# Kernel tuning notes

Hardware: AMD Instinct MI355X
Metric: run time of the kernel (lower is better)

The kernel has to match this reference:

```python
import jax, jax.numpy as jnp
import numpy as np

B, L, D, I = 64, 196, 2048, 512

def setup_inputs() -> dict:
    key = jax.random.key(0)
    ks = jax.random.split(key, 8)
    s_f = 1.0 / np.sqrt(D)
    s_h = 1.0 / np.sqrt(I)
    s_a = 1.0 / np.sqrt(I)
    return {
        "feature_vectors": jax.random.normal(ks[0], (B, L, D), dtype=jnp.float32),
        "hidden_state": jax.random.normal(ks[1], (B, I), dtype=jnp.float32),
        "W_f": jax.random.uniform(ks[2], (D, I), jnp.float32, -s_f, s_f),
        "b_f": jax.random.uniform(ks[3], (I,), jnp.float32, -s_f, s_f),
        "W_h": jax.random.uniform(ks[4], (I, I), jnp.float32, -s_h, s_h),
        "b_h": jax.random.uniform(ks[5], (I,), jnp.float32, -s_h, s_h),
        "W_a": jax.random.uniform(ks[6], (I, D), jnp.float32, -s_a, s_a),
        "b_a": jax.random.uniform(ks[7], (D,), jnp.float32, -s_a, s_a),
    }

def reference(feature_vectors, hidden_state, W_f, b_f, W_h, b_h, W_a, b_a):
    # fv: [B,L,D], hidden: [B,I]
    fv_shaped = jnp.einsum('bld,di->bli', feature_vectors, W_f) + b_f      # [B,L,I]
    hs_shaped = hidden_state @ W_h + b_h                                   # [B,I]
    e = jnp.einsum('bli,id->bld', fv_shaped + hs_shaped[:, None, :], W_a) + b_a  # [B,L,D]
    alpha = jax.nn.softmax(e, axis=1)                                      # softmax over L locations
    z = jnp.sum(alpha * feature_vectors, axis=1)                           # [B,D] (vectorized loop)
    return (z, alpha)
```

## Files before the change

### kernel.cpp

```cpp
#include <hip/hip_runtime.h>

#define B_ 64
#define L_ 196
#define D_ 2048
#define I_ 512
#define M_ (B_*L_)

typedef __attribute__((ext_vector_type(8))) short bf16x8;
typedef __attribute__((ext_vector_type(4))) float f32x4;
typedef unsigned short u16;

__device__ __forceinline__ u16 f2bf(float x){
  unsigned u = __float_as_uint(x);
  u += 0x7fffu + ((u >> 16) & 1u);
  return (u16)(u >> 16);
}

__device__ __forceinline__ void gld16(const void* g, void* l){
  __builtin_amdgcn_global_load_lds(
      (const __attribute__((address_space(1))) void*)g,
      (__attribute__((address_space(3))) void*)l, 16, 0, 0);
}

template<int N> __device__ __forceinline__ void wait_vm(){
  __builtin_amdgcn_s_waitcnt((N&15) | ((N&48)<<10) | (7<<4) | (15<<8));
}
__device__ __forceinline__ void wait_lgkm0(){
  __builtin_amdgcn_s_waitcnt(15 | (48<<10) | (7<<4));
}
__device__ __forceinline__ void bar(){
  asm volatile("" ::: "memory");
  __builtin_amdgcn_s_barrier();
  asm volatile("" ::: "memory");
}

__device__ __forceinline__ unsigned cvtpk(float a, float b){
  unsigned r;
  asm("v_cvt_pk_bf16_f32 %0, %1, %2" : "=v"(r) : "v"(a), "v"(b));
  return r;
}

__global__ void transpose_cvt_kernel(const float* __restrict__ in, u16* __restrict__ out, int R, int C){
  __shared__ float tile[32][33];
  int c0 = blockIdx.x*32, r0 = blockIdx.y*32;
  int tx = threadIdx.x, ty = threadIdx.y;
  for (int i=0;i<32;i+=8)
    tile[ty+i][tx] = in[(size_t)(r0+ty+i)*C + c0 + tx];
  __syncthreads();
  for (int i=0;i<32;i+=8)
    out[(size_t)(c0+ty+i)*R + r0 + tx] = f2bf(tile[tx][ty+i]);
}

__launch_bounds__(256)
__global__ void hs_kernel(const float* __restrict__ hidden, const float* __restrict__ Wh,
                          const float* __restrict__ bh, float* __restrict__ hs){
  __shared__ float red[4][64];
  const int nl = threadIdx.x & 63, kg = threadIdx.x >> 6;
  const int n = blockIdx.x*64 + nl, b = blockIdx.y;
  const float* hrow = hidden + b*I_;
  float a0=0.f, a1=0.f;
  #pragma unroll
  for (int k=kg*128; k<kg*128+128; k+=2){
    a0 = fmaf(hrow[k+0], Wh[(size_t)(k+0)*I_ + n], a0);
    a1 = fmaf(hrow[k+1], Wh[(size_t)(k+1)*I_ + n], a1);
  }
  red[kg][nl] = a0 + a1;
  __syncthreads();
  if (kg == 0)
    hs[b*I_ + n] = bh[n] + (red[0][nl]+red[1][nl]) + (red[2][nl]+red[3][nl]);
}

__launch_bounds__(256)
__global__ void gemm1_kernel(const float* __restrict__ A, const u16* __restrict__ Bt,
                             const float* __restrict__ bias, const float* __restrict__ hs,
                             u16* __restrict__ outb)
{
  constexpr int K = D_, BK = 64, NIT = K/BK;
  __shared__ __align__(16) u16 Als[2][128*64];
  __shared__ __align__(16) u16 Bls[2][64*64];

  const int tid = threadIdx.x, lane = tid&63, wave = tid>>6;
  const int lid = blockIdx.y*8 + blockIdx.x;
  const int wid = (lid & 7)*98 + (lid >> 3);
  const int m0 = (wid >> 3)*128, n0 = (wid & 7)*64;
  const int q = lane>>4, mr = lane&15;
  const int wm = (wave&1)*64, wn = (wave>>1)*32;

  const int a_r  = wave*32 + (lane>>4);
  const int a_kc = lane&15;
  const float* Aw = A + (size_t)(m0 + a_r)*K + a_kc*4;
  const int b_r  = wave*16 + (lane>>3);
  const int b_kc = lane&7;
  const u16* Bw = Bt + (size_t)(n0 + b_r)*K + b_kc*8;

  int awo[8], bwo[2];
  #pragma unroll
  for (int u=0;u<8;++u){
    int r = a_r + u*4;
    awo[u] = r*64 + (((a_kc>>1) ^ (r&7))*8) + (a_kc&1)*4;
  }
  #pragma unroll
  for (int v=0;v<2;++v){
    int r = b_r + v*8;
    bwo[v] = r*64 + ((b_kc ^ (r&7))*8);
  }

  int aro[2][4], bro[2][2];
  #pragma unroll
  for (int s=0;s<2;++s){
    #pragma unroll
    for (int i2=0;i2<4;++i2){
      int r = wm + i2*16 + mr;
      aro[s][i2] = r*64 + (((s*4+q) ^ (r&7))*8);
    }
    #pragma unroll
    for (int j=0;j<2;++j){
      int r = wn + j*16 + mr;
      bro[s][j] = r*64 + (((s*4+q) ^ (r&7))*8);
    }
  }

  f32x4 rA[8]; bf16x8 rB[2];
  f32x4 acc[4][2];
  #pragma unroll
  for (int i=0;i<4;++i)
    #pragma unroll
    for (int j=0;j<2;++j) acc[i][j] = (f32x4){0.f,0.f,0.f,0.f};

#define G1_LOAD(k0) { \
  _Pragma("unroll") \
  for (int u=0;u<8;++u) rA[u] = *(const f32x4*)(Aw + (size_t)(u*4)*K + (k0)); \
  _Pragma("unroll") \
  for (int v=0;v<2;++v) rB[v] = *(const bf16x8*)(Bw + (size_t)(v*8)*K + (k0)); }

#define G1_CVTWR(bi) { \
  u16* Ab_ = Als[bi]; u16* Bb_ = Bls[bi]; \
  _Pragma("unroll") \
  for (int u=0;u<8;++u){ \
    unsigned lo = cvtpk(rA[u][0], rA[u][1]); \
    unsigned hi = cvtpk(rA[u][2], rA[u][3]); \
    *(uint2*)(Ab_ + awo[u]) = make_uint2(lo, hi); \
  } \
  _Pragma("unroll") \
  for (int v=0;v<2;++v) *(bf16x8*)(Bb_ + bwo[v]) = rB[v]; }

  G1_LOAD(0)
  G1_CVTWR(0)
  G1_LOAD(BK)
  wait_lgkm0(); bar();

  for (int t=0; t<NIT; ++t){
    if (t+1 < NIT) G1_CVTWR((t+1)&1)
    if (t+2 < NIT) G1_LOAD((t+2)*BK)
    const u16* Ab = Als[t&1];
    const u16* Bb = Bls[t&1];
    #pragma unroll
    for (int s=0;s<2;++s){
      bf16x8 af[4], bg[2];
      #pragma unroll
      for (int i2=0;i2<4;++i2) af[i2] = *(const bf16x8*)(Ab + aro[s][i2]);
      #pragma unroll
      for (int j=0;j<2;++j)    bg[j]  = *(const bf16x8*)(Bb + bro[s][j]);
      #pragma unroll
      for (int i2=0;i2<4;++i2)
        #pragma unroll
        for (int j=0;j<2;++j)
          acc[i2][j] = __builtin_amdgcn_mfma_f32_16x16x32_bf16(af[i2], bg[j], acc[i2][j], 0,0,0);
    }
    wait_lgkm0();
    bar();
  }

  #pragma unroll
  for (int i2=0;i2<4;++i2){
    #pragma unroll
    for (int j=0;j<2;++j){
      int gcol = n0 + wn + j*16 + mr;
      float bcol = bias[gcol];
      #pragma unroll
      for (int r=0;r<4;++r){
        int grow = m0 + wm + i2*16 + q*4 + r;
        int batch = grow / L_;
        outb[(size_t)grow*I_ + gcol] = f2bf(acc[i2][j][r] + bcol + hs[batch*I_ + gcol]);
      }
    }
  }
#undef G1_LOAD
#undef G1_CVTWR
}

__launch_bounds__(256)
__global__ void gemm2_fused_kernel(const u16* __restrict__ T, const u16* __restrict__ Wa,
                                   const float* __restrict__ b_a, const float* __restrict__ fv,
                                   float* __restrict__ out)
{
  constexpr int K = I_, BK = 32, NIT = K/BK;
  __shared__ __align__(16) u16 Als[2][256*32];
  __shared__ __align__(16) u16 Bls[2][64*32];

  const int tid = threadIdx.x, lane = tid&63, wave = tid>>6;
  const int b = blockIdx.y, n0 = blockIdx.x*64;
  const int q = lane>>4, mr = lane&15;
  const int l16 = lane>>2, kc4 = (lane&3)^(l16&3);

  const u16* Ag[4]; int Alo[4];
  #pragma unroll
  for (int u=0;u<4;++u){
    int j = wave*4+u;
    int grow = b*L_ + j*16 + l16; if (grow > M_-1) grow = M_-1;
    Ag[u] = T + (size_t)grow*K + kc4*8; Alo[u] = j*512;
  }
  const u16* Bg = Wa + (size_t)(n0 + wave*16 + l16)*K + kc4*8;
  const int  Blo = wave*512;

  const int abase = mr*32 + ((q ^ (mr&3))*8);
  const int col  = n0 + wave*16 + mr;
  const int boff = (wave*16+mr)*32 + ((q ^ (mr&3))*8);

  f32x4 acc[13];
  #pragma unroll
  for (int i=0;i<13;i++) acc[i] = (f32x4){0,0,0,0};

  #pragma unroll
  for (int u=0;u<4;++u) gld16(Ag[u],    &Als[0][Alo[u]]);
  gld16(Bg,    &Bls[0][Blo]);
  #pragma unroll
  for (int u=0;u<4;++u) gld16(Ag[u]+BK, &Als[1][Alo[u]]);
  gld16(Bg+BK, &Bls[1][Blo]);

  for (int it=0; it<NIT; ++it){
    if (it+1<NIT) wait_vm<5>(); else wait_vm<0>();
    bar();
    const u16* Ab = Als[it&1];
    const u16* Bb = Bls[it&1];
    bf16x8 bg0 = *(const bf16x8*)(Bb + boff);
    bf16x8 af[13];
    #pragma unroll
    for (int i=0;i<13;++i) af[i] = *(const bf16x8*)(Ab + abase + i*512);
    wait_lgkm0();
    bar();
    if (it+2<NIT){
      int k0 = (it+2)*BK;
      #pragma unroll
      for (int u=0;u<4;++u) gld16(Ag[u]+k0, &Als[it&1][Alo[u]]);
      gld16(Bg+k0, &Bls[it&1][Blo]);
    }
    #pragma unroll
    for (int i=0;i<13;++i)
      acc[i] = __builtin_amdgcn_mfma_f32_16x16x32_bf16(af[i], bg0, acc[i], 0,0,0);
  }

  const bool v12 = (q == 0);
  float bc = b_a[col];
  #pragma unroll
  for (int i=0;i<13;++i)
    #pragma unroll
    for (int r=0;r<4;++r) acc[i][r] += bc;

  float m = -3.4e38f;
  #pragma unroll
  for (int i=0;i<12;++i)
    #pragma unroll
    for (int r=0;r<4;++r) m = fmaxf(m, acc[i][r]);
  if (v12)
    #pragma unroll
    for (int r=0;r<4;++r) m = fmaxf(m, acc[12][r]);
  m = fmaxf(m, __shfl_xor(m, 16));
  m = fmaxf(m, __shfl_xor(m, 32));

  float s = 0.f;
  #pragma unroll
  for (int i=0;i<12;++i)
    #pragma unroll
    for (int r=0;r<4;++r){ float e = __expf(acc[i][r]-m); acc[i][r] = e; s += e; }
  if (v12)
    #pragma unroll
    for (int r=0;r<4;++r){ float e = __expf(acc[12][r]-m); acc[12][r] = e; s += e; }
  s += __shfl_xor(s, 16);
  s += __shfl_xor(s, 32);
  float inv = 1.f/s;

  float* alpha = out + (size_t)B_*D_ + (size_t)b*L_*D_;
  const float* fvb = fv + (size_t)b*L_*D_;
  float z = 0.f;
  #pragma unroll
  for (int i=0;i<13;++i){
    if (i < 12 || v12){
      #pragma unroll
      for (int r=0;r<4;++r){
        int row = i*16 + q*4 + r;
        float a = acc[i][r] * inv;
        alpha[(size_t)row*D_ + col] = a;
        z = fmaf(a, fvb[(size_t)row*D_ + col], z);
      }
    }
  }
  z += __shfl_xor(z, 16);
  z += __shfl_xor(z, 32);
  if (q == 0) out[(size_t)b*D_ + col] = z;
}

extern "C" void kernel_launch(void* const* d_in, const int* in_sizes, int n_in,
                              void* d_out, int out_size, void* d_ws, size_t ws_size,
                              hipStream_t stream){
  (void)in_sizes; (void)n_in; (void)out_size; (void)ws_size;
  const float* fv     = (const float*)d_in[0];
  const float* hidden = (const float*)d_in[1];
  const float* W_f    = (const float*)d_in[2];
  const float* b_f    = (const float*)d_in[3];
  const float* W_h    = (const float*)d_in[4];
  const float* b_h    = (const float*)d_in[5];
  const float* W_a    = (const float*)d_in[6];
  const float* b_a    = (const float*)d_in[7];
  float* out = (float*)d_out;

  char* ws = (char*)d_ws;
  u16*   t_bf  = (u16*)ws;
  u16*   WfT   = (u16*)(ws + 12845056);
  u16*   WaT   = (u16*)(ws + 14942208);
  float* hsbuf = (float*)(ws + 17039360);

  transpose_cvt_kernel<<<dim3(I_/32, D_/32), dim3(32,8), 0, stream>>>(W_f, WfT, D_, I_);
  transpose_cvt_kernel<<<dim3(D_/32, I_/32), dim3(32,8), 0, stream>>>(W_a, WaT, I_, D_);
  hs_kernel<<<dim3(I_/64, B_), 256, 0, stream>>>(hidden, W_h, b_h, hsbuf);

  gemm1_kernel<<<dim3(8, M_/128), 256, 0, stream>>>(fv, WfT, b_f, hsbuf, t_bf);
  gemm2_fused_kernel<<<dim3(D_/64, B_), 256, 0, stream>>>(t_bf, WaT, b_a, fv, out);
}
```

Before: 313.1 us.

## Merge prep kernels into one launch and split gemm1 tile across eight waves

Folds the two weight transpose/convert launches and the hidden-state projection into a single prep kernel that dispatches on block index, removing two kernel launches. gemm1 now uses 512 threads (8 waves) per 128x64 tile, so each wave owns a 32x32 sub-tile and loads half as much per stage. This cuts per-thread registers and adds more waves to hide latency, at the cost of fewer MFMAs per wave between barriers and more barrier participants.

```diff
diff --git a/kernel.cpp b/kernel.cpp
--- a/kernel.cpp
+++ b/kernel.cpp
@@ -40,37 +40,47 @@
   return r;
 }
 
-__global__ void transpose_cvt_kernel(const float* __restrict__ in, u16* __restrict__ out, int R, int C){
+__launch_bounds__(256)
+__global__ void prep_kernel(const float* __restrict__ Wf, u16* __restrict__ WfT,
+                            const float* __restrict__ Wa, u16* __restrict__ WaT,
+                            const float* __restrict__ hidden, const float* __restrict__ Wh,
+                            const float* __restrict__ bh, float* __restrict__ hsbuf){
   __shared__ float tile[32][33];
-  int c0 = blockIdx.x*32, r0 = blockIdx.y*32;
-  int tx = threadIdx.x, ty = threadIdx.y;
-  for (int i=0;i<32;i+=8)
-    tile[ty+i][tx] = in[(size_t)(r0+ty+i)*C + c0 + tx];
-  __syncthreads();
-  for (int i=0;i<32;i+=8)
-    out[(size_t)(c0+ty+i)*R + r0 + tx] = f2bf(tile[tx][ty+i]);
-}
-
-__launch_bounds__(256)
-__global__ void hs_kernel(const float* __restrict__ hidden, const float* __restrict__ Wh,
-                          const float* __restrict__ bh, float* __restrict__ hs){
   __shared__ float red[4][64];
-  const int nl = threadIdx.x & 63, kg = threadIdx.x >> 6;
-  const int n = blockIdx.x*64 + nl, b = blockIdx.y;
-  const float* hrow = hidden + b*I_;
-  float a0=0.f, a1=0.f;
-  #pragma unroll
-  for (int k=kg*128; k<kg*128+128; k+=2){
-    a0 = fmaf(hrow[k+0], Wh[(size_t)(k+0)*I_ + n], a0);
-    a1 = fmaf(hrow[k+1], Wh[(size_t)(k+1)*I_ + n], a1);
-  }
-  red[kg][nl] = a0 + a1;
-  __syncthreads();
-  if (kg == 0)
-    hs[b*I_ + n] = bh[n] + (red[0][nl]+red[1][nl]) + (red[2][nl]+red[3][nl]);
-}
-
-__launch_bounds__(256)
+  const int bid = blockIdx.x, tid = threadIdx.x;
+  if (bid < 2048){
+    const float* in; u16* out; int R, C, id;
+    if (bid < 1024){ in = Wf; out = WfT; R = D_; C = I_; id = bid; }
+    else           { in = Wa; out = WaT; R = I_; C = D_; id = bid - 1024; }
+    const int nx = C/32;
+    const int c0 = (id % nx)*32, r0 = (id / nx)*32;
+    const int tx = tid & 31, ty = tid >> 5;
+    #pragma unroll
+    for (int i=0;i<32;i+=8)
+      tile[ty+i][tx] = in[(size_t)(r0+ty+i)*C + c0 + tx];
+    __syncthreads();
+    #pragma unroll
+    for (int i=0;i<32;i+=8)
+      out[(size_t)(c0+ty+i)*R + r0 + tx] = f2bf(tile[tx][ty+i]);
+  } else {
+    const int id = bid - 2048;
+    const int nl = tid & 63, kg = tid >> 6;
+    const int n = (id & 7)*64 + nl, b = id >> 3;
+    const float* hrow = hidden + b*I_;
+    float a0=0.f, a1=0.f;
+    #pragma unroll
+    for (int k=kg*128; k<kg*128+128; k+=2){
+      a0 = fmaf(hrow[k+0], Wh[(size_t)(k+0)*I_ + n], a0);
+      a1 = fmaf(hrow[k+1], Wh[(size_t)(k+1)*I_ + n], a1);
+    }
+    red[kg][nl] = a0 + a1;
+    __syncthreads();
+    if (kg == 0)
+      hsbuf[b*I_ + n] = bh[n] + (red[0][nl]+red[1][nl]) + (red[2][nl]+red[3][nl]);
+  }
+}
+
+__launch_bounds__(512)
 __global__ void gemm1_kernel(const float* __restrict__ A, const u16* __restrict__ Bt,
                              const float* __restrict__ bias, const float* __restrict__ hs,
                              u16* __restrict__ outb)
@@ -84,32 +94,28 @@
   const int wid = (lid & 7)*98 + (lid >> 3);
   const int m0 = (wid >> 3)*128, n0 = (wid & 7)*64;
   const int q = lane>>4, mr = lane&15;
-  const int wm = (wave&1)*64, wn = (wave>>1)*32;
-
-  const int a_r  = wave*32 + (lane>>4);
+  const int wm = (wave&3)*32, wn = (wave>>2)*32;
+
+  const int a_r  = wave*16 + (lane>>4);
   const int a_kc = lane&15;
   const float* Aw = A + (size_t)(m0 + a_r)*K + a_kc*4;
-  const int b_r  = wave*16 + (lane>>3);
+  const int b_r  = wave*8 + (lane>>3);
   const int b_kc = lane&7;
   const u16* Bw = Bt + (size_t)(n0 + b_r)*K + b_kc*8;
 
-  int awo[8], bwo[2];
-  #pragma unroll
-  for (int u=0;u<8;++u){
+  int awo[4];
+  #pragma unroll
+  for (int u=0;u<4;++u){
     int r = a_r + u*4;
     awo[u] = r*64 + (((a_kc>>1) ^ (r&7))*8) + (a_kc&1)*4;
   }
-  #pragma unroll
-  for (int v=0;v<2;++v){
-    int r = b_r + v*8;
-    bwo[v] = r*64 + ((b_kc ^ (r&7))*8);
-  }
-
-  int aro[2][4], bro[2][2];
+  const int bwo = b_r*64 + ((b_kc ^ (b_r&7))*8);
+
+  int aro[2][2], bro[2][2];
   #pragma unroll
   for (int s=0;s<2;++s){
     #pragma unroll
-    for (int i2=0;i2<4;++i2){
+    for (int i2=0;i2<2;++i2){
       int r = wm + i2*16 + mr;
       aro[s][i2] = r*64 + (((s*4+q) ^ (r&7))*8);
     }
@@ -120,29 +126,27 @@
     }
   }
 
-  f32x4 rA[8]; bf16x8 rB[2];
-  f32x4 acc[4][2];
-  #pragma unroll
-  for (int i=0;i<4;++i)
+  f32x4 rA[4]; bf16x8 rB;
+  f32x4 acc[2][2];
+  #pragma unroll
+  for (int i=0;i<2;++i)
     #pragma unroll
     for (int j=0;j<2;++j) acc[i][j] = (f32x4){0.f,0.f,0.f,0.f};
 
 #define G1_LOAD(k0) { \
   _Pragma("unroll") \
-  for (int u=0;u<8;++u) rA[u] = *(const f32x4*)(Aw + (size_t)(u*4)*K + (k0)); \
-  _Pragma("unroll") \
-  for (int v=0;v<2;++v) rB[v] = *(const bf16x8*)(Bw + (size_t)(v*8)*K + (k0)); }
+  for (int u=0;u<4;++u) rA[u] = *(const f32x4*)(Aw + (size_t)(u*4)*K + (k0)); \
+  rB = *(const bf16x8*)(Bw + (k0)); }
 
 #define G1_CVTWR(bi) { \
   u16* Ab_ = Als[bi]; u16* Bb_ = Bls[bi]; \
   _Pragma("unroll") \
-  for (int u=0;u<8;++u){ \
+  for (int u=0;u<4;++u){ \
     unsigned lo = cvtpk(rA[u][0], rA[u][1]); \
     unsigned hi = cvtpk(rA[u][2], rA[u][3]); \
     *(uint2*)(Ab_ + awo[u]) = make_uint2(lo, hi); \
   } \
-  _Pragma("unroll") \
-  for (int v=0;v<2;++v) *(bf16x8*)(Bb_ + bwo[v]) = rB[v]; }
+  *(bf16x8*)(Bb_ + bwo) = rB; }
 
   G1_LOAD(0)
   G1_CVTWR(0)
@@ -156,13 +160,13 @@
     const u16* Bb = Bls[t&1];
     #pragma unroll
     for (int s=0;s<2;++s){
-      bf16x8 af[4], bg[2];
-      #pragma unroll
-      for (int i2=0;i2<4;++i2) af[i2] = *(const bf16x8*)(Ab + aro[s][i2]);
+      bf16x8 af[2], bg[2];
+      #pragma unroll
+      for (int i2=0;i2<2;++i2) af[i2] = *(const bf16x8*)(Ab + aro[s][i2]);
       #pragma unroll
       for (int j=0;j<2;++j)    bg[j]  = *(const bf16x8*)(Bb + bro[s][j]);
       #pragma unroll
-      for (int i2=0;i2<4;++i2)
+      for (int i2=0;i2<2;++i2)
         #pragma unroll
         for (int j=0;j<2;++j)
           acc[i2][j] = __builtin_amdgcn_mfma_f32_16x16x32_bf16(af[i2], bg[j], acc[i2][j], 0,0,0);
@@ -172,7 +176,7 @@
   }
 
   #pragma unroll
-  for (int i2=0;i2<4;++i2){
+  for (int i2=0;i2<2;++i2){
     #pragma unroll
     for (int j=0;j<2;++j){
       int gcol = n0 + wn + j*16 + mr;
@@ -320,10 +324,7 @@
   u16*   WaT   = (u16*)(ws + 14942208);
   float* hsbuf = (float*)(ws + 17039360);
 
-  transpose_cvt_kernel<<<dim3(I_/32, D_/32), dim3(32,8), 0, stream>>>(W_f, WfT, D_, I_);
-  transpose_cvt_kernel<<<dim3(D_/32, I_/32), dim3(32,8), 0, stream>>>(W_a, WaT, I_, D_);
-  hs_kernel<<<dim3(I_/64, B_), 256, 0, stream>>>(hidden, W_h, b_h, hsbuf);
-
-  gemm1_kernel<<<dim3(8, M_/128), 256, 0, stream>>>(fv, WfT, b_f, hsbuf, t_bf);
+  prep_kernel<<<2560, 256, 0, stream>>>(W_f, WfT, W_a, WaT, hidden, W_h, b_h, hsbuf);
+  gemm1_kernel<<<dim3(8, M_/128), 512, 0, stream>>>(fv, WfT, b_f, hsbuf, t_bf);
   gemm2_fused_kernel<<<dim3(D_/64, B_), 256, 0, stream>>>(t_bf, WaT, b_a, fv, out);
 }
```

After: 316.0 us. No clear change (+0.9%).
